# Performance work log

Hardware: AMD Instinct MI355X
Metric: run time of the kernel (lower is better)

Reference implementation:

```python
import jax, jax.numpy as jnp
import numpy as np

B, S, D = 2, 2048, 1024
H, DH = 16, 64
N_CTX = 2048
IGNORE = -100000.0


def setup_inputs() -> dict:
    key = jax.random.key(0)
    ks = jax.random.split(key, 6)
    scale = 0.02
    return {
        "x": jax.random.normal(ks[0], (B, S, D), dtype=jnp.float32),
        "W_Q": jax.random.normal(ks[1], (H, DH, D), dtype=jnp.float32) * scale,
        "W_K": jax.random.normal(ks[2], (H, DH, D), dtype=jnp.float32) * scale,
        "W_V": jax.random.normal(ks[3], (H, DH, D), dtype=jnp.float32) * scale,
        "W_O": jax.random.normal(ks[4], (H, D, DH), dtype=jnp.float32) * scale,
        "b_Q": jnp.zeros((H, DH), dtype=jnp.float32),
        "b_K": jnp.zeros((H, DH), dtype=jnp.float32),
        "b_V": jnp.zeros((H, DH), dtype=jnp.float32),
        "b_O": jnp.zeros((D,), dtype=jnp.float32),
    }


def reference(x, W_Q, W_K, W_V, W_O, b_Q, b_K, b_V, b_O):
    attn_scale = jnp.sqrt(jnp.asarray(DH, dtype=x.dtype))
    # q,k,v: [batch, pos, head, d_head]
    q = jnp.einsum('ihm,bpm->bpih', W_Q, x) + b_Q
    k = jnp.einsum('ihm,bpm->bpih', W_K, x) + b_K
    v = jnp.einsum('ihm,bpm->bpih', W_V, x) + b_V
    # scores: [batch, head, q_pos, k_pos]
    attn_scores = jnp.einsum('bpih,bqih->bipq', q, k) / attn_scale
    # causal mask (pos_start=0, no kv cache)
    qs, ks_ = attn_scores.shape[-2], attn_scores.shape[-1]
    mask = jnp.tril(jnp.ones((qs, ks_), dtype=bool))
    attn_scores = jnp.where(mask, attn_scores, jnp.asarray(IGNORE, dtype=attn_scores.dtype))
    attn_matrix = jax.nn.softmax(attn_scores, axis=-1)
    # z: [batch, q_pos, head, d_head]
    z = jnp.einsum('bpih,biqp->bqih', v, attn_matrix)
    out = jnp.einsum('idh,bqih->bqd', W_O, z) + b_O
    return out
```

## Files before the change

kernel.cpp:

```cpp
#include <hip/hip_runtime.h>

typedef __bf16 bf16;
typedef __bf16 bf16x4 __attribute__((ext_vector_type(4)));
typedef __bf16 bf16x8 __attribute__((ext_vector_type(8)));
typedef float f32x4 __attribute__((ext_vector_type(4)));
typedef unsigned u32x4 __attribute__((ext_vector_type(4)));

#define AS1C(p) ((const __attribute__((address_space(1))) void*)(p))
#define AS3(p)  ((__attribute__((address_space(3))) void*)(p))

__device__ __forceinline__ void gld16(const bf16* gsrc, bf16* ldst) {
  __builtin_amdgcn_global_load_lds(AS1C(gsrc), AS3(ldst), 16, 0, 0);
}


__global__ void castx_kernel(const float* __restrict__ x, bf16* __restrict__ xb) {
  const int n4 = (4096 * 1024) / 4;
  for (int i = blockIdx.x * blockDim.x + threadIdx.x; i < n4; i += gridDim.x * blockDim.x) {
    float4 v = ((const float4*)x)[i];
    bf16x4 o;
    o[0] = (bf16)v.x; o[1] = (bf16)v.y; o[2] = (bf16)v.z; o[3] = (bf16)v.w;
    ((bf16x4*)xb)[i] = o;
  }
}

__global__ void prep_kernel(const float* __restrict__ WQ, const float* __restrict__ WK,
                            const float* __restrict__ WV, const float* __restrict__ WO,
                            const float* __restrict__ bQ, const float* __restrict__ bK,
                            const float* __restrict__ bV,
                            bf16* __restrict__ Wqkv, bf16* __restrict__ Wo2,
                            float* __restrict__ biasq) {
  const int WN = 1024 * 1024;
  const int total = 4 * WN + 3072;
  for (int i = blockIdx.x * blockDim.x + threadIdx.x; i < total; i += gridDim.x * blockDim.x) {
    if (i < WN) {
      Wqkv[i] = (bf16)(WQ[i] * 0.125f);
    } else if (i < 2 * WN) {
      Wqkv[i] = (bf16)WK[i - WN];
    } else if (i < 3 * WN) {
      Wqkv[i] = (bf16)WV[i - 2 * WN];
    } else if (i < 4 * WN) {
      int j = i - 3 * WN;
      int hh = j >> 16, r = j & 65535, d = r >> 6, dh = r & 63;
      Wo2[d * 1024 + hh * 64 + dh] = (bf16)WO[j];
    } else {
      int n = i - 4 * WN;
      biasq[n] = (n < 1024) ? bQ[n] * 0.125f : (n < 2048) ? bK[n - 1024] : bV[n - 2048];
    }
  }
}

template <int MODE>
__global__ __launch_bounds__(256)
void gemm_bt(const bf16* __restrict__ A, const bf16* __restrict__ Bw,
             const float* __restrict__ bias,
             bf16* __restrict__ Qo, bf16* __restrict__ Ko, bf16* __restrict__ Vt,
             float* __restrict__ Co, int M, int N, int K) {
  __shared__ bf16 As[128 * 64];
  __shared__ bf16 Bs[128 * 64];
  const int tid = threadIdx.x;
  const int lane = tid & 63, w = tid >> 6;
  const int wr = w >> 1, wc = w & 1;
  const int g = lane >> 4, lr = lane & 15;
  const int brow = blockIdx.x * 128, bcol = blockIdx.y * 128;

  f32x4 acc[4][4] = {};

  for (int k0 = 0; k0 < K; k0 += 64) {
#pragma unroll
    for (int it = 0; it < 4; ++it) {
      const int chunk = it * 4 + w;
      const int e = chunk * 64 + lane;
      const int row = e >> 3;
      const int c8 = (e & 7) << 3;
      gld16(A + (size_t)(brow + row) * K + k0 + c8, As + chunk * 512);
      gld16(Bw + (size_t)(bcol + row) * K + k0 + c8, Bs + chunk * 512);
    }
    __syncthreads();
#pragma unroll
    for (int kk = 0; kk < 2; ++kk) {
      bf16x8 af[4], bfm[4];
#pragma unroll
      for (int m = 0; m < 4; ++m)
        af[m] = *(const bf16x8*)(As + (wr * 64 + m * 16 + lr) * 64 + kk * 32 + g * 8);
#pragma unroll
      for (int n = 0; n < 4; ++n)
        bfm[n] = *(const bf16x8*)(Bs + (wc * 64 + n * 16 + lr) * 64 + kk * 32 + g * 8);
#pragma unroll
      for (int m = 0; m < 4; ++m)
#pragma unroll
        for (int n = 0; n < 4; ++n)
          acc[m][n] = __builtin_amdgcn_mfma_f32_16x16x32_bf16(af[m], bfm[n], acc[m][n], 0, 0, 0);
    }
    __syncthreads();
  }

  const int row0 = brow + wr * 64;
  const int col0 = bcol + wc * 64;
#pragma unroll
  for (int m = 0; m < 4; ++m) {
#pragma unroll
    for (int n = 0; n < 4; ++n) {
      const int nidx = col0 + n * 16 + lr;
      f32x4 v = acc[m][n];
      const float bs = bias[nidx];
      if (MODE == 0) {
        const int stream = nidx >> 10;
        const int j = nidx & 1023;
        const int hh = j >> 6, dh = j & 63;
        const int r0 = row0 + m * 16 + g * 4;
        const int b = r0 >> 11;
        const int p0 = r0 & 2047;
        if (stream == 2) {
          bf16x4 vv;
#pragma unroll
          for (int i = 0; i < 4; ++i) vv[i] = (bf16)(v[i] + bs);
          *(bf16x4*)(Vt + ((size_t)(b * 16 + hh) * 64 + dh) * 2048 + p0) = vv;
        } else {
          bf16* dst = (stream == 0) ? Qo : Ko;
#pragma unroll
          for (int i = 0; i < 4; ++i)
            dst[((size_t)(b * 16 + hh) * 2048 + (p0 + i)) * 64 + dh] = (bf16)(v[i] + bs);
        }
      } else {
#pragma unroll
        for (int i = 0; i < 4; ++i) {
          const int r = row0 + m * 16 + g * 4 + i;
          Co[(size_t)r * 1024 + nidx] = v[i] + bs;
        }
      }
    }
  }
}

__global__ __launch_bounds__(256, 4)
void attn_kernel(const bf16* __restrict__ Qm, const bf16* __restrict__ Km,
                 const bf16* __restrict__ Vm, bf16* __restrict__ Z,
                 bf16* __restrict__ OP, float2* __restrict__ ML) {
  const int nblk = blockIdx.x;
  const int xcd = nblk & 7, s2 = nblk >> 3;
  const int Gl = s2 & 3, u = s2 >> 2;
  const int G = Gl * 8 + xcd;
  const int hh = G & 15, b = G >> 4;
  const int lane = threadIdx.x & 63, w = threadIdx.x >> 6;
  const int g = lane >> 4, lr = lane & 15;
  const bool g0 = g & 1, g1 = (g >> 1) & 1;

  int qt, t0, t1, spl;
  if (u < 32) {
    qt = 31 - (u >> 1); spl = u & 1;
    const int T = qt + 1, mid = (T + 1) >> 1;
    t0 = spl ? mid : 0; t1 = spl ? T : mid;
  } else {
    qt = 47 - u; spl = -1; t0 = 0; t1 = qt + 1;
  }

  __shared__ bf16 Ks[2][4096];
  __shared__ bf16 Vs[2][4096];

  const bf16* Qb = Qm + (size_t)G * 2048 * 64;
  const bf16* Kb = Km + (size_t)G * 2048 * 64;
  const bf16* Vb = Vm + (size_t)G * 64 * 2048;

  auto stage = [&](int kv0, int bufi) {
#pragma unroll
    for (int it = 0; it < 2; ++it) {
      const int cb = w * 128 + it * 64;
      const int uu = cb + lane;
      const int lc = uu ^ ((uu >> 3) & 7);
      const int row = lc >> 3, c8 = (lc & 7) * 8;
      gld16(Kb + (size_t)(kv0 + row) * 64 + c8, &Ks[bufi][cb * 8]);
      gld16(Vb + (size_t)row * 2048 + kv0 + c8, &Vs[bufi][cb * 8]);
    }
  };

  const int q0w = qt * 64 + w * 16;
  const int qg = q0w + lr;

  bf16x8 aq[2];
#pragma unroll
  for (int kk = 0; kk < 2; ++kk)
    aq[kk] = *(const bf16x8*)(Qb + (size_t)qg * 64 + kk * 32 + g * 8);

  float m_i = -1e30f, l_i = 0.f;
  f32x4 oacc[4] = {};

  int buf = 0;
  stage(t0 * 64, 0);
  __syncthreads();

  for (int t = t0; t < t1; ++t) {
    if (t + 1 < t1) stage((t + 1) * 64, buf ^ 1);
    const int kv0 = t * 64;

    f32x4 s[4] = {};
#pragma unroll
    for (int kk = 0; kk < 2; ++kk) {
#pragma unroll
      for (int n = 0; n < 4; ++n) {
        const int r = n * 16 + lr;
        const int sl = (r * 8 + kk * 4 + g) ^ (r & 7);
        bf16x8 bk = *(const bf16x8*)(&Ks[buf][sl * 8]);
        s[n] = __builtin_amdgcn_mfma_f32_16x16x32_bf16(bk, aq[kk], s[n], 0, 0, 0);
      }
    }
    if (t == qt) {
#pragma unroll
      for (int n = 0; n < 4; ++n)
#pragma unroll
        for (int i = 0; i < 4; ++i)
          if (kv0 + n * 16 + g * 4 + i > qg) s[n][i] = -1e9f;
    }

    float tm = fmaxf(fmaxf(fmaxf(s[0][0], s[0][1]), fmaxf(s[0][2], s[0][3])),
                     fmaxf(fmaxf(s[1][0], s[1][1]), fmaxf(s[1][2], s[1][3])));
    tm = fmaxf(tm, fmaxf(fmaxf(fmaxf(s[2][0], s[2][1]), fmaxf(s[2][2], s[2][3])),
                         fmaxf(fmaxf(s[3][0], s[3][1]), fmaxf(s[3][2], s[3][3]))));
    tm = fmaxf(tm, __shfl_xor(tm, 16));
    tm = fmaxf(tm, __shfl_xor(tm, 32));
    const float mn = fmaxf(m_i, tm);
    const float al = __expf(m_i - mn);
    m_i = mn;
#pragma unroll
    for (int n = 0; n < 4; ++n)
#pragma unroll
      for (int i = 0; i < 4; ++i) s[n][i] = __expf(s[n][i] - mn);
    float ts = ((s[0][0] + s[0][1]) + (s[0][2] + s[0][3])) +
               ((s[1][0] + s[1][1]) + (s[1][2] + s[1][3])) +
               ((s[2][0] + s[2][1]) + (s[2][2] + s[2][3])) +
               ((s[3][0] + s[3][1]) + (s[3][2] + s[3][3]));
    ts += __shfl_xor(ts, 16);
    ts += __shfl_xor(ts, 32);
    l_i = l_i * al + ts;
#pragma unroll
    for (int n = 0; n < 4; ++n)
#pragma unroll
      for (int i = 0; i < 4; ++i) oacc[n][i] *= al;

    unsigned U[8];
#pragma unroll
    for (int n = 0; n < 4; ++n)
#pragma unroll
      for (int h = 0; h < 2; ++h) {
        unsigned lo = (unsigned)__builtin_bit_cast(unsigned short, (bf16)s[n][2 * h]);
        unsigned hi = (unsigned)__builtin_bit_cast(unsigned short, (bf16)s[n][2 * h + 1]);
        U[n * 2 + h] = lo | (hi << 16);
      }
    unsigned rA0 = (unsigned)__shfl_xor((int)(g1 ? U[0] : U[2]), 32);
    unsigned rA1 = (unsigned)__shfl_xor((int)(g1 ? U[1] : U[3]), 32);
    unsigned rA2 = (unsigned)__shfl_xor((int)(g1 ? U[4] : U[6]), 32);
    unsigned rA3 = (unsigned)__shfl_xor((int)(g1 ? U[5] : U[7]), 32);
    unsigned v2_000 = g1 ? rA0 : U[0];
    unsigned v2_001 = g1 ? rA1 : U[1];
    unsigned v2_010 = g1 ? U[2] : rA0;
    unsigned v2_011 = g1 ? U[3] : rA1;
    unsigned v2_100 = g1 ? rA2 : U[4];
    unsigned v2_101 = g1 ? rA3 : U[5];
    unsigned v2_110 = g1 ? U[6] : rA2;
    unsigned v2_111 = g1 ? U[7] : rA3;
    unsigned rB0 = (unsigned)__shfl_xor((int)(g0 ? v2_000 : v2_010), 16);
    unsigned rB1 = (unsigned)__shfl_xor((int)(g0 ? v2_001 : v2_011), 16);
    unsigned rB2 = (unsigned)__shfl_xor((int)(g0 ? v2_100 : v2_110), 16);
    unsigned rB3 = (unsigned)__shfl_xor((int)(g0 ? v2_101 : v2_111), 16);
    u32x4 t0v, t1v;
    t0v[0] = g0 ? rB0 : v2_000;
    t0v[1] = g0 ? rB1 : v2_001;
    t0v[2] = g0 ? v2_010 : rB0;
    t0v[3] = g0 ? v2_011 : rB1;
    t1v[0] = g0 ? rB2 : v2_100;
    t1v[1] = g0 ? rB3 : v2_101;
    t1v[2] = g0 ? v2_110 : rB2;
    t1v[3] = g0 ? v2_111 : rB3;
    bf16x8 pb0 = __builtin_bit_cast(bf16x8, t0v);
    bf16x8 pb1 = __builtin_bit_cast(bf16x8, t1v);

#pragma unroll
    for (int kk = 0; kk < 2; ++kk) {
      const bf16x8 pb = kk ? pb1 : pb0;
#pragma unroll
      for (int n = 0; n < 4; ++n) {
        const int r = n * 16 + lr;
        const int sl = (r * 8 + kk * 4 + g) ^ (r & 7);
        bf16x8 av = *(const bf16x8*)(&Vs[buf][sl * 8]);
        oacc[n] = __builtin_amdgcn_mfma_f32_16x16x32_bf16(av, pb, oacc[n], 0, 0, 0);
      }
    }
    __syncthreads();
    buf ^= 1;
  }

  if (u < 32) {
    const int pr = G * 1024 + (qt - 16) * 64 + w * 16 + lr;
    bf16* oprow = OP + (size_t)(spl * 32768 + pr) * 64;
#pragma unroll
    for (int n = 0; n < 4; ++n) {
      bf16x4 o4;
#pragma unroll
      for (int i = 0; i < 4; ++i) o4[i] = (bf16)oacc[n][i];
      *(bf16x4*)(oprow + n * 16 + g * 4) = o4;
    }
    if (lane < 16) ML[spl * 32768 + pr] = make_float2(m_i, l_i);
  } else {
    const float li = 1.f / l_i;
    bf16* zrow = Z + ((size_t)(b * 2048 + qg) * 16 + hh) * 64;
#pragma unroll
    for (int n = 0; n < 4; ++n) {
      bf16x4 o4;
#pragma unroll
      for (int i = 0; i < 4; ++i) o4[i] = (bf16)(oacc[n][i] * li);
      *(bf16x4*)(zrow + n * 16 + g * 4) = o4;
    }
  }
}

__global__ __launch_bounds__(256)
void combine_kernel(const bf16* __restrict__ OP, const float2* __restrict__ ML,
                    bf16* __restrict__ Z) {
  const int id = blockIdx.x * 256 + threadIdx.x;
  const int pr = id >> 3, d8 = id & 7;
  const float2 ml0 = ML[pr], ml1 = ML[32768 + pr];
  const float m = fmaxf(ml0.x, ml1.x);
  const float w0 = __expf(ml0.x - m), w1 = __expf(ml1.x - m);
  const float inv = 1.f / (ml0.y * w0 + ml1.y * w1);
  const bf16x8 a = *(const bf16x8*)(OP + (size_t)pr * 64 + d8 * 8);
  const bf16x8 c = *(const bf16x8*)(OP + ((size_t)32768 + pr) * 64 + d8 * 8);
  bf16x8 o;
#pragma unroll
  for (int j = 0; j < 8; ++j)
    o[j] = (bf16)(((float)a[j] * w0 + (float)c[j] * w1) * inv);
  const int bh = pr >> 10, qr = pr & 1023;
  const int bb = bh >> 4, hq = bh & 15;
  *(bf16x8*)(Z + (((size_t)(bb * 2048 + 1024 + qr)) * 16 + hq) * 64 + d8 * 8) = o;
}

extern "C" void kernel_launch(void* const* d_in, const int* in_sizes, int n_in,
                              void* d_out, int out_size, void* d_ws, size_t ws_size,
                              hipStream_t stream) {
  const float* x  = (const float*)d_in[0];
  const float* WQ = (const float*)d_in[1];
  const float* WK = (const float*)d_in[2];
  const float* WV = (const float*)d_in[3];
  const float* WO = (const float*)d_in[4];
  const float* bQ = (const float*)d_in[5];
  const float* bK = (const float*)d_in[6];
  const float* bV = (const float*)d_in[7];
  const float* bO = (const float*)d_in[8];
  float* out = (float*)d_out;

  char* ws = (char*)d_ws;
  bf16* xb    = (bf16*)(ws);
  bf16* Wqkv  = (bf16*)(ws + (8u << 20));
  bf16* Wo2   = (bf16*)(ws + (14u << 20));
  bf16* Qb    = (bf16*)(ws + (16u << 20));
  bf16* Kb    = (bf16*)(ws + (24u << 20));
  bf16* Vtb   = (bf16*)(ws + (32u << 20));
  bf16* Zb    = (bf16*)(ws + (40u << 20));
  float* biasq = (float*)(ws + (48u << 20));
  bf16* OP    = (bf16*)(ws);
  float2* ML  = (float2*)(ws + (8u << 20));

  castx_kernel<<<2048, 256, 0, stream>>>(x, xb);
  prep_kernel<<<2048, 256, 0, stream>>>(WQ, WK, WV, WO, bQ, bK, bV, Wqkv, Wo2, biasq);
  gemm_bt<0><<<dim3(32, 24), 256, 0, stream>>>(xb, Wqkv, biasq, Qb, Kb, Vtb, nullptr,
                                               4096, 3072, 1024);
  attn_kernel<<<1536, 256, 0, stream>>>(Qb, Kb, Vtb, Zb, OP, ML);
  combine_kernel<<<1024, 256, 0, stream>>>(OP, ML, Zb);
  gemm_bt<1><<<dim3(32, 8), 256, 0, stream>>>(Zb, Wo2, bO, nullptr, nullptr, nullptr, out,
                                              4096, 1024, 1024);
}
```

Before: 221.5 us.

## Double-buffer GEMM LDS tiles with XOR swizzle and grouped tile ordering

Result: faster. 207.4 us (-6.4%).

```diff
diff --git a/kernel.cpp b/kernel.cpp
--- a/kernel.cpp
+++ b/kernel.cpp
@@ -51,48 +51,63 @@
 }
 
 template <int MODE>
-__global__ __launch_bounds__(256)
+__global__ __launch_bounds__(256, 2)
 void gemm_bt(const bf16* __restrict__ A, const bf16* __restrict__ Bw,
              const float* __restrict__ bias,
              bf16* __restrict__ Qo, bf16* __restrict__ Ko, bf16* __restrict__ Vt,
              float* __restrict__ Co, int M, int N, int K) {
-  __shared__ bf16 As[128 * 64];
-  __shared__ bf16 Bs[128 * 64];
+  __shared__ bf16 As[2][8192];
+  __shared__ bf16 Bs[2][8192];
   const int tid = threadIdx.x;
   const int lane = tid & 63, w = tid >> 6;
   const int wr = w >> 1, wc = w & 1;
   const int g = lane >> 4, lr = lane & 15;
-  const int brow = blockIdx.x * 128, bcol = blockIdx.y * 128;
+  const int perx = gridDim.x >> 3;
+  const int tile = (blockIdx.x & 7) * perx + (blockIdx.x >> 3);
+  const int brow = (tile & 31) * 128, bcol = (tile >> 5) * 128;
+
+  auto stage = [&](int k0, int bufi) {
+#pragma unroll
+    for (int it = 0; it < 4; ++it) {
+      const int cb = (it * 4 + w) * 64;
+      const int u = cb + lane;
+      const int lc = u ^ ((u >> 3) & 7);
+      const int row = lc >> 3, c8 = (lc & 7) * 8;
+      gld16(A + (size_t)(brow + row) * K + k0 + c8, &As[bufi][cb * 8]);
+      gld16(Bw + (size_t)(bcol + row) * K + k0 + c8, &Bs[bufi][cb * 8]);
+    }
+  };
 
   f32x4 acc[4][4] = {};
-
-  for (int k0 = 0; k0 < K; k0 += 64) {
-#pragma unroll
-    for (int it = 0; it < 4; ++it) {
-      const int chunk = it * 4 + w;
-      const int e = chunk * 64 + lane;
-      const int row = e >> 3;
-      const int c8 = (e & 7) << 3;
-      gld16(A + (size_t)(brow + row) * K + k0 + c8, As + chunk * 512);
-      gld16(Bw + (size_t)(bcol + row) * K + k0 + c8, Bs + chunk * 512);
-    }
+  stage(0, 0);
+  const int nstep = K >> 6;
+
+  for (int t = 0; t < nstep; ++t) {
     __syncthreads();
+    if (t + 1 < nstep) stage((t + 1) << 6, (t + 1) & 1);
+    const bf16* as = As[t & 1];
+    const bf16* bs = Bs[t & 1];
 #pragma unroll
     for (int kk = 0; kk < 2; ++kk) {
       bf16x8 af[4], bfm[4];
 #pragma unroll
-      for (int m = 0; m < 4; ++m)
-        af[m] = *(const bf16x8*)(As + (wr * 64 + m * 16 + lr) * 64 + kk * 32 + g * 8);
-#pragma unroll
-      for (int n = 0; n < 4; ++n)
-        bfm[n] = *(const bf16x8*)(Bs + (wc * 64 + n * 16 + lr) * 64 + kk * 32 + g * 8);
+      for (int m = 0; m < 4; ++m) {
+        const int row = wr * 64 + m * 16 + lr;
+        const int sl = (row * 8 + kk * 4 + g) ^ (lr & 7);
+        af[m] = *(const bf16x8*)(as + sl * 8);
+      }
+#pragma unroll
+      for (int n = 0; n < 4; ++n) {
+        const int row = wc * 64 + n * 16 + lr;
+        const int sl = (row * 8 + kk * 4 + g) ^ (lr & 7);
+        bfm[n] = *(const bf16x8*)(bs + sl * 8);
+      }
 #pragma unroll
       for (int m = 0; m < 4; ++m)
 #pragma unroll
         for (int n = 0; n < 4; ++n)
           acc[m][n] = __builtin_amdgcn_mfma_f32_16x16x32_bf16(af[m], bfm[n], acc[m][n], 0, 0, 0);
     }
-    __syncthreads();
   }
 
   const int row0 = brow + wr * 64;
@@ -361,10 +376,10 @@
 
   castx_kernel<<<2048, 256, 0, stream>>>(x, xb);
   prep_kernel<<<2048, 256, 0, stream>>>(WQ, WK, WV, WO, bQ, bK, bV, Wqkv, Wo2, biasq);
-  gemm_bt<0><<<dim3(32, 24), 256, 0, stream>>>(xb, Wqkv, biasq, Qb, Kb, Vtb, nullptr,
-                                               4096, 3072, 1024);
+  gemm_bt<0><<<768, 256, 0, stream>>>(xb, Wqkv, biasq, Qb, Kb, Vtb, nullptr,
+                                      4096, 3072, 1024);
   attn_kernel<<<1536, 256, 0, stream>>>(Qb, Kb, Vtb, Zb, OP, ML);
   combine_kernel<<<1024, 256, 0, stream>>>(OP, ML, Zb);
-  gemm_bt<1><<<dim3(32, 8), 256, 0, stream>>>(Zb, Wo2, bO, nullptr, nullptr, nullptr, out,
-                                              4096, 1024, 1024);
-}
+  gemm_bt<1><<<256, 256, 0, stream>>>(Zb, Wo2, bO, nullptr, nullptr, nullptr, out,
+                                      4096, 1024, 1024);
+}
```
